# Performance work log

Hardware: AMD Instinct MI355X
Metric: run time of the kernel (lower is better)

Reference implementation:

```python
import jax, jax.numpy as jnp
import numpy as np

DIM = 1024
NHEAD = 16
HEAD_DIM = DIM // NHEAD


def setup_inputs() -> dict:
    key = jax.random.key(0)
    k_x, k_wqkv, k_bqkv, k_wp, k_bp = jax.random.split(key, 5)
    scale = 1.0 / np.sqrt(DIM)
    return {
        "x": jax.random.normal(k_x, (4, 2048, DIM), dtype=jnp.float32),
        "w_qkv": jax.random.uniform(k_wqkv, (DIM, 3 * DIM), minval=-scale, maxval=scale, dtype=jnp.float32),
        "b_qkv": jax.random.uniform(k_bqkv, (3 * DIM,), minval=-scale, maxval=scale, dtype=jnp.float32),
        "w_proj": jax.random.uniform(k_wp, (DIM, DIM), minval=-scale, maxval=scale, dtype=jnp.float32),
        "b_proj": jax.random.uniform(k_bp, (DIM,), minval=-scale, maxval=scale, dtype=jnp.float32),
    }


def reference(x, w_qkv, b_qkv, w_proj, b_proj):
    B, N, D = x.shape
    # qkv projection: [B,N,3D] -> [3,B,H,N,hd]
    qkv = x @ w_qkv + b_qkv
    qkv = qkv.reshape(B, N, 3, NHEAD, HEAD_DIM).transpose(2, 0, 3, 1, 4)
    q, k, v = qkv[0], qkv[1], qkv[2]
    # naive full attention: scores [B,H,N,N]
    attn = jnp.einsum("bhqd,bhkd->bhqk", q, k) / jnp.sqrt(jnp.float32(HEAD_DIM))
    attn = jax.nn.softmax(attn, axis=-1)
    out = jnp.einsum("bhqk,bhkd->bhqd", attn, v)  # [B,H,N,hd]
    out = out.transpose(0, 2, 1, 3).reshape(B, N, D)
    return out @ w_proj + b_proj
```

## Files before the change

kernel.cpp:

```cpp
#include <hip/hip_runtime.h>
#include <math.h>

#define DIM     1024
#define NHEAD   16
#define HD      64
#define BATCH   4
#define SEQ     2048
#define MTOT    (BATCH * SEQ)
#define QKV_N   (3 * DIM)

typedef __attribute__((ext_vector_type(8))) short bf16x8;
typedef __attribute__((ext_vector_type(4))) float f32x4;
typedef unsigned int u32;
typedef unsigned short u16;

__device__ __forceinline__ u16 f2bf(float f) {
    u32 u = __float_as_uint(f);
    return (u16)((u + 0x7fffu + ((u >> 16) & 1u)) >> 16);
}

__device__ __forceinline__ float exp2_fast(float x) {
    float r; asm("v_exp_f32 %0, %1" : "=v"(r) : "v"(x)); return r;
}

__device__ __forceinline__ u32 cvtpk_bf16(float lo, float hi) {
    u32 r; asm("v_cvt_pk_bf16_f32 %0, %1, %2" : "=v"(r) : "v"(lo), "v"(hi));
    return r;
}

__device__ __forceinline__ void gload_lds16(const u16* g, u16* l) {
    __builtin_amdgcn_global_load_lds((const __attribute__((address_space(1))) u32*)g,
                                     (__attribute__((address_space(3))) u32*)l, 16, 0, 0);
}

__global__ __launch_bounds__(256) void cast_x(const float* __restrict__ in,
                                              u16* __restrict__ out) {
    const int i = (blockIdx.x * 256 + threadIdx.x) * 4;
    const float4 v = *(const float4*)&in[i];
    ushort4 o;
    o.x = f2bf(v.x); o.y = f2bf(v.y); o.z = f2bf(v.z); o.w = f2bf(v.w);
    *(ushort4*)&out[i] = o;
}

__global__ __launch_bounds__(256) void cast_transpose(const float* __restrict__ W,
                                                      u16* __restrict__ Wt,
                                                      int K, int N) {
    __shared__ float Ls[64][65];
    const int k0 = blockIdx.x * 64, n0 = blockIdx.y * 64;
    const int t = threadIdx.x;
    const int r = t >> 4, c4 = (t & 15) << 2;
    #pragma unroll
    for (int i = 0; i < 4; ++i) {
        const float4 v = *(const float4*)&W[(size_t)(k0 + r + i * 16) * N + n0 + c4];
        Ls[r + i * 16][c4 + 0] = v.x; Ls[r + i * 16][c4 + 1] = v.y;
        Ls[r + i * 16][c4 + 2] = v.z; Ls[r + i * 16][c4 + 3] = v.w;
    }
    __syncthreads();
    #pragma unroll
    for (int i = 0; i < 4; ++i) {
        const int nr = r + i * 16;
        ushort4 o;
        o.x = f2bf(Ls[c4 + 0][nr]); o.y = f2bf(Ls[c4 + 1][nr]);
        o.z = f2bf(Ls[c4 + 2][nr]); o.w = f2bf(Ls[c4 + 3][nr]);
        *(ushort4*)&Wt[(size_t)(n0 + nr) * K + k0 + c4] = o;
    }
}

#define GEMM_MAINLOOP(Aptr, Bptr)                                              \
    __shared__ __align__(16) u16 As[128 * 32];                                 \
    __shared__ __align__(16) u16 Bs[128 * 32];                                 \
    const int t = threadIdx.x;                                                 \
    const int lane = t & 63, w = t >> 6;                                       \
    const int nwg = gridDim.x * gridDim.y;                                     \
    int flat = blockIdx.y * gridDim.x + blockIdx.x;                            \
    flat = (flat & 7) * (nwg >> 3) + (flat >> 3);                              \
    const int n0 = (flat % gridDim.x) * 128;                                   \
    const int m0 = (flat / gridDim.x) * 128;                                   \
    const int wm = (w & 1) * 64, wn = (w >> 1) * 64;                           \
    const int g = lane >> 4, li = lane & 15;                                   \
    f32x4 acc[4][4];                                                           \
    _Pragma("unroll") for (int mt = 0; mt < 4; ++mt)                           \
        _Pragma("unroll") for (int nt = 0; nt < 4; ++nt)                       \
            acc[mt][nt] = (f32x4){0.f, 0.f, 0.f, 0.f};                         \
    for (int k0 = 0; k0 < DIM; k0 += 32) {                                     \
        _Pragma("unroll") for (int i = 0; i < 2; ++i) {                        \
            const int row = w * 32 + i * 16 + (lane >> 2);                     \
            const int slot = (lane & 3) ^ ((row >> 1) & 3);                    \
            gload_lds16(&Aptr[(size_t)(m0 + row) * DIM + k0 + slot * 8],       \
                        &As[(w * 32 + i * 16) * 32]);                          \
            gload_lds16(&Bptr[(size_t)(n0 + row) * DIM + k0 + slot * 8],       \
                        &Bs[(w * 32 + i * 16) * 32]);                          \
        }                                                                      \
        __syncthreads();                                                       \
        bf16x8 a[4], b[4];                                                     \
        _Pragma("unroll") for (int mt = 0; mt < 4; ++mt) {                     \
            const int row = wm + mt * 16 + li;                                 \
            const int slot = g ^ ((row >> 1) & 3);                             \
            a[mt] = *(const bf16x8*)&As[row * 32 + slot * 8];                  \
        }                                                                      \
        _Pragma("unroll") for (int nt = 0; nt < 4; ++nt) {                     \
            const int row = wn + nt * 16 + li;                                 \
            const int slot = g ^ ((row >> 1) & 3);                             \
            b[nt] = *(const bf16x8*)&Bs[row * 32 + slot * 8];                  \
        }                                                                      \
        _Pragma("unroll") for (int mt = 0; mt < 4; ++mt)                       \
            _Pragma("unroll") for (int nt = 0; nt < 4; ++nt)                   \
                acc[mt][nt] = __builtin_amdgcn_mfma_f32_16x16x32_bf16(         \
                    a[mt], b[nt], acc[mt][nt], 0, 0, 0);                       \
        __syncthreads();                                                       \
    }

#define QSCALE 0.18033688011112042f
__global__ __launch_bounds__(256) void gemm_qkv(
    const u16* __restrict__ A, const u16* __restrict__ Bt,
    const float* __restrict__ bias,
    u16* __restrict__ qo, u16* __restrict__ ko, u16* __restrict__ vo)
{
    GEMM_MAINLOOP(A, Bt)
    #pragma unroll
    for (int nt = 0; nt < 4; ++nt) {
        const int n = n0 + wn + nt * 16 + li;
        const int which = n >> 10;
        const int head  = (n >> 6) & 15;
        const int hd    = n & 63;
        u16* dst = (which == 0) ? qo : (which == 1) ? ko : vo;
        const float scale = (which == 0) ? QSCALE : 1.0f;
        const float bv = bias[n];
        #pragma unroll
        for (int mt = 0; mt < 4; ++mt) {
            #pragma unroll
            for (int r = 0; r < 4; ++r) {
                const int m = m0 + wm + mt * 16 + g * 4 + r;
                const int bb = m >> 11, tok = m & 2047;
                dst[((size_t)(bb * NHEAD + head) * SEQ + tok) * HD + hd] =
                    f2bf((acc[mt][nt][r] + bv) * scale);
            }
        }
    }
}

__global__ __launch_bounds__(256) void gemm_proj(
    const u16* __restrict__ A, const u16* __restrict__ Bt,
    const float* __restrict__ bias, float* __restrict__ out)
{
    GEMM_MAINLOOP(A, Bt)
    #pragma unroll
    for (int nt = 0; nt < 4; ++nt) {
        const int n = n0 + wn + nt * 16 + li;
        const float bv = bias[n];
        #pragma unroll
        for (int mt = 0; mt < 4; ++mt) {
            #pragma unroll
            for (int r = 0; r < 4; ++r) {
                const int m = m0 + wm + mt * 16 + g * 4 + r;
                out[(size_t)m * DIM + n] = acc[mt][nt][r] + bv;
            }
        }
    }
}

#define LSTR 72
#define NKT  (SEQ / 64)
__global__ __launch_bounds__(256) void attn_mfma(
    const u16* __restrict__ q, const u16* __restrict__ k,
    const u16* __restrict__ v, u16* __restrict__ ao)
{
    __shared__ __align__(16) u16 Ks[64 * LSTR];
    __shared__ __align__(16) u16 Vt[64 * LSTR];
    __shared__ __align__(16) u16 Ps[4 * 32 * LSTR];

    const int t = threadIdx.x;
    const int lane = t & 63, w = t >> 6;
    const int g = lane >> 4, li = lane & 15;
    const int q0 = blockIdx.x * 128;
    const int bh = blockIdx.y;
    const size_t base = (size_t)bh * SEQ * HD;

    bf16x8 qf[2][2];
    #pragma unroll
    for (int h = 0; h < 2; ++h) {
        const size_t qrow = base + (size_t)(q0 + w * 32 + h * 16 + li) * HD;
        qf[h][0] = *(const bf16x8*)&q[qrow + g * 8];
        qf[h][1] = *(const bf16x8*)&q[qrow + 32 + g * 8];
    }

    float lsum[2] = {0.f, 0.f};
    f32x4 oacc[2][4];
    #pragma unroll
    for (int h = 0; h < 2; ++h)
        #pragma unroll
        for (int nt = 0; nt < 4; ++nt) oacc[h][nt] = (f32x4){0.f, 0.f, 0.f, 0.f};

    u16* Pw = &Ps[w * 32 * LSTR];

    const int kk = t >> 2,        kh  = (t & 3) << 4;
    const int vkey = (t & 31) << 1, vh0 = (t >> 5) << 3;

    bf16x8 rk0, rk1, rv0, rv1;
    {
        const size_t kb = base;
        rk0 = *(const bf16x8*)&k[kb + (size_t)kk * HD + kh];
        rk1 = *(const bf16x8*)&k[kb + (size_t)kk * HD + kh + 8];
        rv0 = *(const bf16x8*)&v[kb + (size_t)vkey * HD + vh0];
        rv1 = *(const bf16x8*)&v[kb + (size_t)(vkey + 1) * HD + vh0];
    }

    for (int kt = 0; kt < NKT; ++kt) {
        *(bf16x8*)&Ks[kk * LSTR + kh]     = rk0;
        *(bf16x8*)&Ks[kk * LSTR + kh + 8] = rk1;
        #pragma unroll
        for (int i = 0; i < 8; ++i) {
            const u32 pk = (u32)(u16)rv0[i] | ((u32)(u16)rv1[i] << 16);
            *(u32*)&Vt[(vh0 + i) * LSTR + vkey] = pk;
        }
        __syncthreads();

        if (kt + 1 < NKT) {
            const size_t kb = base + (size_t)(kt + 1) * 64 * HD;
            rk0 = *(const bf16x8*)&k[kb + (size_t)kk * HD + kh];
            rk1 = *(const bf16x8*)&k[kb + (size_t)kk * HD + kh + 8];
            rv0 = *(const bf16x8*)&v[kb + (size_t)vkey * HD + vh0];
            rv1 = *(const bf16x8*)&v[kb + (size_t)(vkey + 1) * HD + vh0];
        }

        #pragma unroll
        for (int h = 0; h < 2; ++h) {
            f32x4 s[4];
            #pragma unroll
            for (int nt = 0; nt < 4; ++nt) {
                const bf16x8 kf0 = *(const bf16x8*)&Ks[(nt * 16 + li) * LSTR + g * 8];
                const bf16x8 kf1 = *(const bf16x8*)&Ks[(nt * 16 + li) * LSTR + 32 + g * 8];
                f32x4 c = (f32x4){0.f, 0.f, 0.f, 0.f};
                c = __builtin_amdgcn_mfma_f32_16x16x32_bf16(kf0, qf[h][0], c, 0, 0, 0);
                c = __builtin_amdgcn_mfma_f32_16x16x32_bf16(kf1, qf[h][1], c, 0, 0, 0);
                s[nt] = c;
            }
            float rs = 0.f;
            #pragma unroll
            for (int nt = 0; nt < 4; ++nt)
                #pragma unroll
                for (int r = 0; r < 4; ++r) {
                    const float p = exp2_fast(s[nt][r]);
                    s[nt][r] = p;
                    rs += p;
                }
            lsum[h] += rs;
            #pragma unroll
            for (int nt = 0; nt < 4; ++nt) {
                uint2 w2;
                w2.x = cvtpk_bf16(s[nt][0], s[nt][1]);
                w2.y = cvtpk_bf16(s[nt][2], s[nt][3]);
                *(uint2*)&Pw[(h * 16 + li) * LSTR + nt * 16 + (g << 2)] = w2;
            }
        }

        asm volatile("s_waitcnt lgkmcnt(0)" ::: "memory");
        __builtin_amdgcn_sched_barrier(0);

        #pragma unroll
        for (int ks = 0; ks < 2; ++ks) {
            bf16x8 vb[4];
            #pragma unroll
            for (int nt = 0; nt < 4; ++nt)
                vb[nt] = *(const bf16x8*)&Vt[(nt * 16 + li) * LSTR + ks * 32 + g * 8];
            #pragma unroll
            for (int h = 0; h < 2; ++h) {
                const bf16x8 pa = *(const bf16x8*)&Pw[(h * 16 + li) * LSTR + ks * 32 + g * 8];
                #pragma unroll
                for (int nt = 0; nt < 4; ++nt)
                    oacc[h][nt] = __builtin_amdgcn_mfma_f32_16x16x32_bf16(
                        pa, vb[nt], oacc[h][nt], 0, 0, 0);
            }
        }
        __syncthreads();
    }

    const int bb = bh >> 4, hd = bh & 15;
    #pragma unroll
    for (int h = 0; h < 2; ++h) {
        float lf = lsum[h];
        lf += __shfl_xor(lf, 16);
        lf += __shfl_xor(lf, 32);
        #pragma unroll
        for (int r = 0; r < 4; ++r) {
            const float lr = __shfl(lf, (lane & 48) + (g << 2) + r);
            const float inv = 1.0f / lr;
            const int tok = q0 + w * 32 + h * 16 + (g << 2) + r;
            #pragma unroll
            for (int nt = 0; nt < 4; ++nt)
                ao[((size_t)(bb * SEQ + tok)) * DIM + hd * HD + nt * 16 + li] =
                    f2bf(oacc[h][nt][r] * inv);
        }
    }
}

extern "C" void kernel_launch(void* const* d_in, const int* in_sizes, int n_in,
                              void* d_out, int out_size, void* d_ws, size_t ws_size,
                              hipStream_t stream)
{
    const float* x      = (const float*)d_in[0];
    const float* w_qkv  = (const float*)d_in[1];
    const float* b_qkv  = (const float*)d_in[2];
    const float* w_proj = (const float*)d_in[3];
    const float* b_proj = (const float*)d_in[4];
    float* out = (float*)d_out;

    u16* xb  = (u16*)d_ws;
    u16* wqt = xb  + (size_t)MTOT * DIM;
    u16* wpt = wqt + (size_t)QKV_N * DIM;
    u16* qb  = wpt + (size_t)DIM * DIM;
    u16* kb  = qb  + (size_t)MTOT * DIM;
    u16* vb  = kb  + (size_t)MTOT * DIM;
    u16* aob = vb  + (size_t)MTOT * DIM;

    cast_x<<<(MTOT * DIM) / 1024, 256, 0, stream>>>(x, xb);
    cast_transpose<<<dim3(DIM / 64, QKV_N / 64), 256, 0, stream>>>(w_qkv, wqt, DIM, QKV_N);
    cast_transpose<<<dim3(DIM / 64, DIM / 64), 256, 0, stream>>>(w_proj, wpt, DIM, DIM);

    gemm_qkv<<<dim3(QKV_N / 128, MTOT / 128), 256, 0, stream>>>(xb, wqt, b_qkv, qb, kb, vb);
    attn_mfma<<<dim3(SEQ / 128, BATCH * NHEAD), 256, 0, stream>>>(qb, kb, vb, aob);
    gemm_proj<<<dim3(DIM / 128, MTOT / 128), 256, 0, stream>>>(aob, wpt, b_proj, out);
}
```

Before: 218.7 us.

## Double-buffer GEMM LDS tiles, drop grid swizzle, reorder attention QK loop with setprio

The GEMM main loop now uses two LDS buffers, prefetching the next K-slice with global-to-LDS loads while computing on the current one, so one barrier per iteration is removed. The XCD-aware block-index swizzle is dropped in favour of plain blockIdx mapping, which may hurt L2 locality across chiplets. In the attention kernel the QK^T loop is reordered so each K fragment is loaded once and reused for both query halves, and s_setprio raises wave priority around the MFMA blocks. The LDS footprint of the GEMM doubles.

```diff
diff --git a/kernel.cpp b/kernel.cpp
--- a/kernel.cpp
+++ b/kernel.cpp
@@ -66,48 +66,51 @@
     }
 }
 
+#define GEMM_STAGE(buf, kof, Aptr, Bptr)                                       \
+    _Pragma("unroll") for (int i = 0; i < 2; ++i) {                            \
+        const int row = w * 32 + i * 16 + (lane >> 2);                         \
+        const int slot = (lane & 3) ^ ((row >> 1) & 3);                        \
+        gload_lds16(&Aptr[(size_t)(m0 + row) * DIM + (kof) + slot * 8],        \
+                    &As[buf][(w * 32 + i * 16) * 32]);                         \
+        gload_lds16(&Bptr[(size_t)(n0 + row) * DIM + (kof) + slot * 8],        \
+                    &Bs[buf][(w * 32 + i * 16) * 32]);                         \
+    }
+
 #define GEMM_MAINLOOP(Aptr, Bptr)                                              \
-    __shared__ __align__(16) u16 As[128 * 32];                                 \
-    __shared__ __align__(16) u16 Bs[128 * 32];                                 \
+    __shared__ __align__(16) u16 As[2][128 * 32];                              \
+    __shared__ __align__(16) u16 Bs[2][128 * 32];                              \
     const int t = threadIdx.x;                                                 \
     const int lane = t & 63, w = t >> 6;                                       \
-    const int nwg = gridDim.x * gridDim.y;                                     \
-    int flat = blockIdx.y * gridDim.x + blockIdx.x;                            \
-    flat = (flat & 7) * (nwg >> 3) + (flat >> 3);                              \
-    const int n0 = (flat % gridDim.x) * 128;                                   \
-    const int m0 = (flat / gridDim.x) * 128;                                   \
+    const int n0 = blockIdx.x * 128;                                           \
+    const int m0 = blockIdx.y * 128;                                           \
     const int wm = (w & 1) * 64, wn = (w >> 1) * 64;                           \
     const int g = lane >> 4, li = lane & 15;                                   \
     f32x4 acc[4][4];                                                           \
     _Pragma("unroll") for (int mt = 0; mt < 4; ++mt)                           \
         _Pragma("unroll") for (int nt = 0; nt < 4; ++nt)                       \
             acc[mt][nt] = (f32x4){0.f, 0.f, 0.f, 0.f};                         \
+    GEMM_STAGE(0, 0, Aptr, Bptr)                                               \
+    __syncthreads();                                                           \
+    int cur = 0;                                                               \
     for (int k0 = 0; k0 < DIM; k0 += 32) {                                     \
-        _Pragma("unroll") for (int i = 0; i < 2; ++i) {                        \
-            const int row = w * 32 + i * 16 + (lane >> 2);                     \
-            const int slot = (lane & 3) ^ ((row >> 1) & 3);                    \
-            gload_lds16(&Aptr[(size_t)(m0 + row) * DIM + k0 + slot * 8],       \
-                        &As[(w * 32 + i * 16) * 32]);                          \
-            gload_lds16(&Bptr[(size_t)(n0 + row) * DIM + k0 + slot * 8],       \
-                        &Bs[(w * 32 + i * 16) * 32]);                          \
-        }                                                                      \
-        __syncthreads();                                                       \
+        if (k0 + 32 < DIM) { GEMM_STAGE(cur ^ 1, k0 + 32, Aptr, Bptr) }        \
         bf16x8 a[4], b[4];                                                     \
         _Pragma("unroll") for (int mt = 0; mt < 4; ++mt) {                     \
             const int row = wm + mt * 16 + li;                                 \
             const int slot = g ^ ((row >> 1) & 3);                             \
-            a[mt] = *(const bf16x8*)&As[row * 32 + slot * 8];                  \
+            a[mt] = *(const bf16x8*)&As[cur][row * 32 + slot * 8];             \
         }                                                                      \
         _Pragma("unroll") for (int nt = 0; nt < 4; ++nt) {                     \
             const int row = wn + nt * 16 + li;                                 \
             const int slot = g ^ ((row >> 1) & 3);                             \
-            b[nt] = *(const bf16x8*)&Bs[row * 32 + slot * 8];                  \
+            b[nt] = *(const bf16x8*)&Bs[cur][row * 32 + slot * 8];             \
         }                                                                      \
         _Pragma("unroll") for (int mt = 0; mt < 4; ++mt)                       \
             _Pragma("unroll") for (int nt = 0; nt < 4; ++nt)                   \
                 acc[mt][nt] = __builtin_amdgcn_mfma_f32_16x16x32_bf16(         \
                     a[mt], b[nt], acc[mt][nt], 0, 0, 0);                       \
         __syncthreads();                                                       \
+        cur ^= 1;                                                              \
     }
 
 #define QSCALE 0.18033688011112042f
@@ -223,33 +226,39 @@
             rv1 = *(const bf16x8*)&v[kb + (size_t)(vkey + 1) * HD + vh0];
         }
 
-        #pragma unroll
-        for (int h = 0; h < 2; ++h) {
-            f32x4 s[4];
-            #pragma unroll
-            for (int nt = 0; nt < 4; ++nt) {
-                const bf16x8 kf0 = *(const bf16x8*)&Ks[(nt * 16 + li) * LSTR + g * 8];
-                const bf16x8 kf1 = *(const bf16x8*)&Ks[(nt * 16 + li) * LSTR + 32 + g * 8];
+        f32x4 s[2][4];
+        __builtin_amdgcn_s_setprio(1);
+        #pragma unroll
+        for (int nt = 0; nt < 4; ++nt) {
+            const bf16x8 kf0 = *(const bf16x8*)&Ks[(nt * 16 + li) * LSTR + g * 8];
+            const bf16x8 kf1 = *(const bf16x8*)&Ks[(nt * 16 + li) * LSTR + 32 + g * 8];
+            #pragma unroll
+            for (int h = 0; h < 2; ++h) {
                 f32x4 c = (f32x4){0.f, 0.f, 0.f, 0.f};
                 c = __builtin_amdgcn_mfma_f32_16x16x32_bf16(kf0, qf[h][0], c, 0, 0, 0);
                 c = __builtin_amdgcn_mfma_f32_16x16x32_bf16(kf1, qf[h][1], c, 0, 0, 0);
-                s[nt] = c;
-            }
+                s[h][nt] = c;
+            }
+        }
+        __builtin_amdgcn_s_setprio(0);
+
+        #pragma unroll
+        for (int h = 0; h < 2; ++h) {
             float rs = 0.f;
             #pragma unroll
             for (int nt = 0; nt < 4; ++nt)
                 #pragma unroll
                 for (int r = 0; r < 4; ++r) {
-                    const float p = exp2_fast(s[nt][r]);
-                    s[nt][r] = p;
+                    const float p = exp2_fast(s[h][nt][r]);
+                    s[h][nt][r] = p;
                     rs += p;
                 }
             lsum[h] += rs;
             #pragma unroll
             for (int nt = 0; nt < 4; ++nt) {
                 uint2 w2;
-                w2.x = cvtpk_bf16(s[nt][0], s[nt][1]);
-                w2.y = cvtpk_bf16(s[nt][2], s[nt][3]);
+                w2.x = cvtpk_bf16(s[h][nt][0], s[h][nt][1]);
+                w2.y = cvtpk_bf16(s[h][nt][2], s[h][nt][3]);
                 *(uint2*)&Pw[(h * 16 + li) * LSTR + nt * 16 + (g << 2)] = w2;
             }
         }
@@ -257,6 +266,7 @@
         asm volatile("s_waitcnt lgkmcnt(0)" ::: "memory");
         __builtin_amdgcn_sched_barrier(0);
 
+        __builtin_amdgcn_s_setprio(1);
         #pragma unroll
         for (int ks = 0; ks < 2; ++ks) {
             bf16x8 vb[4];
@@ -272,6 +282,7 @@
                         pa, vb[nt], oacc[h][nt], 0, 0, 0);
             }
         }
+        __builtin_amdgcn_s_setprio(0);
         __syncthreads();
     }
 
```

New measurement: 217.3 us. No clear change (-0.6%).
